# Kernel tuning notes

Hardware: AMD Instinct MI355X
Metric: run time of the kernel (lower is better)

The kernel has to match this reference:

```python
import jax, jax.numpy as jnp
import numpy as np

H = 16
D = 64
WIN = 512
THETA = 10000.0


def _rope(x):
    # x: [B, H, T, D]
    T = x.shape[2]
    inv = 1.0 / (THETA ** (jnp.arange(0, D, 2, dtype=jnp.float32) / D))  # [D/2]
    f = jnp.arange(T, dtype=jnp.float32)[:, None] * inv[None, :]          # [T, D/2]
    f = jnp.concatenate([f, f], axis=-1)                                  # [T, D]
    cos, sin = jnp.cos(f), jnp.sin(f)
    x1, x2 = jnp.split(x, 2, axis=-1)
    rot = jnp.concatenate([-x2, x1], axis=-1)
    return x * cos + rot * sin


def setup_inputs() -> dict:
    key = jax.random.key(0)
    ks = jax.random.split(key, 9)
    C = H * D
    s = 0.02
    return {
        "x":  jax.random.normal(ks[0], (2, 2048, C), dtype=jnp.float32),
        "Wq": jax.random.normal(ks[1], (C, C), dtype=jnp.float32) * s,
        "bq": jnp.zeros((C,), dtype=jnp.float32),
        "Wk": jax.random.normal(ks[2], (C, C), dtype=jnp.float32) * s,
        "bk": jnp.zeros((C,), dtype=jnp.float32),
        "Wv": jax.random.normal(ks[3], (C, C), dtype=jnp.float32) * s,
        "bv": jnp.zeros((C,), dtype=jnp.float32),
        "Wo": jax.random.normal(ks[4], (C, C), dtype=jnp.float32) * s,
        "bo": jnp.zeros((C,), dtype=jnp.float32),
    }


def reference(x, Wq, bq, Wk, bk, Wv, bv, Wo, bo):
    B, T, C = x.shape
    def split_heads(y):
        return y.reshape(B, T, H, D).transpose(0, 2, 1, 3)  # [B,H,T,D]
    q = split_heads(x @ Wq + bq)
    k = split_heads(x @ Wk + bk)
    v = split_heads(x @ Wv + bv)
    q = _rope(q)
    k = _rope(k)
    scores = jnp.einsum('bhqd,bhkd->bhqk', q, k) * (1.0 / np.sqrt(D))
    # the original module does NOT apply a causal mask, only the window).
    idx = jnp.arange(T)
    allowed = idx[None, :] >= idx[:, None] - (WIN - 1)      # [T, T] bool
    scores = jnp.where(allowed[None, None], scores, -jnp.inf)
    attn = jax.nn.softmax(scores, axis=-1)
    out = jnp.einsum('bhqk,bhkd->bhqd', attn, v)
    out = out.transpose(0, 2, 1, 3).reshape(B, T, C)
    return out @ Wo + bo
```

## Files before the change

kernel.cpp:

```cpp
#include <hip/hip_runtime.h>
#include <hip/hip_bf16.h>
#include <math.h>

#define Bsz 2
#define Tt  2048
#define Cc  1024
#define Hh  16
#define Dd  64

typedef __attribute__((ext_vector_type(8))) short short8v;
typedef __attribute__((ext_vector_type(4))) short short4v;
typedef __attribute__((ext_vector_type(8))) _Float16 half8v;
typedef __attribute__((ext_vector_type(4))) float f32x4;
typedef __attribute__((ext_vector_type(16))) float f32x16;
typedef __attribute__((ext_vector_type(4))) unsigned int uint4v;

static __device__ __forceinline__ short f2h(float f) {
  _Float16 h = (_Float16)f;
  return __builtin_bit_cast(short, h);
}
static __device__ __forceinline__ float h2f(short s) {
  _Float16 h = __builtin_bit_cast(_Float16, s);
  return (float)h;
}
static __device__ __forceinline__ void gll16(const void* g, void* l) {
  __builtin_amdgcn_global_load_lds((const __attribute__((address_space(1))) unsigned int*)g,
                                   (__attribute__((address_space(3))) unsigned int*)l, 16, 0, 0);
}

__global__ void cast_x(const float* __restrict__ x, short* __restrict__ xh) {
  int t = blockIdx.x * 256 + threadIdx.x;
  const float* s = x + (size_t)t * 8;
  float4 a = *(const float4*)s, b = *(const float4*)(s + 4);
  short8v h;
  h[0] = f2h(a.x); h[1] = f2h(a.y); h[2] = f2h(a.z); h[3] = f2h(a.w);
  h[4] = f2h(b.x); h[5] = f2h(b.y); h[6] = f2h(b.z); h[7] = f2h(b.w);
  *(short8v*)(xh + (size_t)t * 8) = h;
}

__global__ __launch_bounds__(256) void cast_wT(const float* __restrict__ Wq,
                                               const float* __restrict__ Wk,
                                               const float* __restrict__ Wv,
                                               const float* __restrict__ Wo,
                                               short* __restrict__ WTh) {
  __shared__ float T[64][68];
  const int z = blockIdx.z;
  const float* W = z == 0 ? Wq : z == 1 ? Wk : z == 2 ? Wv : Wo;
  short* oh = WTh + (size_t)z * 1048576;
  const int n0 = blockIdx.x * 64, k0 = blockIdx.y * 64;
  const int tid = threadIdx.x;
#pragma unroll
  for (int i = 0; i < 4; ++i) {
    int slot = tid + i * 256;
    int r = slot >> 4, c4 = (slot & 15) << 2;
    *(float4*)&T[r][c4] = *(const float4*)(W + (size_t)(k0 + r) * Cc + n0 + c4);
  }
  __syncthreads();
#pragma unroll
  for (int i = 0; i < 2; ++i) {
    int slot = tid + i * 256;
    int nl = slot >> 3, ks = (slot & 7) << 3;
    short8v h;
#pragma unroll
    for (int e = 0; e < 8; ++e) h[e] = f2h(T[ks + e][nl]);
    *(short8v*)(oh + (size_t)(n0 + nl) * Cc + k0 + ks) = h;
  }
}

__device__ __forceinline__ void core128h(const short* __restrict__ Ah,
                                         const short* __restrict__ Bh,
                                         short* AhL, short* BhL,
                                         int row0, int col0, int wv, int lane, f32x4 acc[4][4]) {
  const int l15 = lane & 15, g = lane >> 4;
  const int wr = wv >> 1, wc = wv & 1;

  const int srow0 = wv * 32 + (lane >> 2);
  const int srow1 = srow0 + 16;
  const int sch0 = ((lane & 3) ^ ((lane >> 2) & 3)) << 3;
  const size_t aoff0 = (size_t)(row0 + srow0) * Cc + sch0;
  const size_t aoff1 = (size_t)(row0 + srow1) * Cc + sch0;
  const size_t boff0 = (size_t)(col0 + srow0) * Cc + sch0;
  const size_t boff1 = (size_t)(col0 + srow1) * Cc + sch0;
  short* dA0 = AhL + wv * 1024;  short* dA1 = dA0 + 512;
  short* dB0 = BhL + wv * 1024;  short* dB1 = dB0 + 512;

  int aL[4], bL[4];
#pragma unroll
  for (int m = 0; m < 4; ++m) aL[m] = (wr * 64 + m * 16 + l15) * 32 + ((g ^ (l15 & 3)) << 3);
#pragma unroll
  for (int n = 0; n < 4; ++n) bL[n] = (wc * 64 + n * 16 + l15) * 32 + ((g ^ (l15 & 3)) << 3);

  for (int k0 = 0; k0 < Cc; k0 += 32) {
    __syncthreads();
    gll16(Ah + aoff0 + k0, dA0);
    gll16(Ah + aoff1 + k0, dA1);
    gll16(Bh + boff0 + k0, dB0);
    gll16(Bh + boff1 + k0, dB1);
    __syncthreads();
    half8v a[4], b[4];
#pragma unroll
    for (int m = 0; m < 4; ++m) a[m] = __builtin_bit_cast(half8v, *(short8v*)&AhL[aL[m]]);
#pragma unroll
    for (int n = 0; n < 4; ++n) b[n] = __builtin_bit_cast(half8v, *(short8v*)&BhL[bL[n]]);
#pragma unroll
    for (int m = 0; m < 4; ++m)
#pragma unroll
      for (int n = 0; n < 4; ++n)
        acc[m][n] = __builtin_amdgcn_mfma_f32_16x16x32_f16(a[m], b[n], acc[m][n], 0, 0, 0);
  }
}

__global__ __launch_bounds__(256, 3) void gemm_qkv(const short* __restrict__ xh,
                                                   const short* __restrict__ WTh,
                                                   const float* __restrict__ bq,
                                                   const float* __restrict__ bk,
                                                   const float* __restrict__ bv,
                                                   short* __restrict__ qb,
                                                   short* __restrict__ kb,
                                                   short* __restrict__ vb) {
  __shared__ short AhL[4096], BhL[4096];
  const int mode = blockIdx.y;
  const short* Bh = WTh + (size_t)mode * 1048576;
  const float* bias = mode == 0 ? bq : mode == 1 ? bk : bv;
  short* Y = mode == 0 ? qb : mode == 1 ? kb : vb;

  const int bid = blockIdx.x;
  const int nid = ((bid & 7) << 5) | (bid >> 3);
  const int row0 = (nid >> 3) * 128, col0 = (nid & 7) * 128;
  const int lane = threadIdx.x & 63, wv = threadIdx.x >> 6;
  const int l15 = lane & 15, g = lane >> 4;
  const int wr = wv >> 1, wc = wv & 1;

  f32x4 acc[4][4];
#pragma unroll
  for (int m = 0; m < 4; ++m)
#pragma unroll
    for (int n = 0; n < 4; ++n) acc[m][n] = (f32x4){0.f, 0.f, 0.f, 0.f};

  core128h(xh, Bh, AhL, BhL, row0, col0, wv, lane, acc);

  const int cbase = col0 + wc * 64;
  const int h = cbase >> 6;
  if (mode < 2) {
    const float scale = (mode == 0) ? 0.18033688f : 1.0f;
#pragma unroll
    for (int n = 0; n < 2; ++n) {
      const int d = n * 16 + l15;
      const float b0 = bias[cbase + d], b1 = bias[cbase + d + 32];
      const float inv = exp2f(-(float)d * (13.2877123795494f / 32.f));
#pragma unroll
      for (int m = 0; m < 4; ++m)
#pragma unroll
        for (int rr = 0; rr < 4; ++rr) {
          int R = row0 + wr * 64 + m * 16 + g * 4 + rr;
          int bI = R >> 11, t = R & (Tt - 1);
          float sn, cs;
          sincosf((float)t * inv, &sn, &cs);
          float v0 = acc[m][n][rr] + b0, v1 = acc[m][n + 2][rr] + b1;
          size_t base = (((size_t)(bI * Hh + h) * Tt + t) << 6) + d;
          Y[base]      = f2h((v0 * cs - v1 * sn) * scale);
          Y[base + 32] = f2h((v1 * cs + v0 * sn) * scale);
        }
    }
  } else {
#pragma unroll
    for (int n = 0; n < 2; ++n) {
      const int d = n * 16 + l15;
      const float b0 = bias[cbase + d], b1 = bias[cbase + d + 32];
#pragma unroll
      for (int m = 0; m < 4; ++m) {
        int R = row0 + wr * 64 + m * 16 + g * 4;
        int bI = R >> 11, t = R & (Tt - 1);
        short4v s0, s1;
#pragma unroll
        for (int rr = 0; rr < 4; ++rr) {
          s0[rr] = f2h(acc[m][n][rr] + b0);
          s1[rr] = f2h(acc[m][n + 2][rr] + b1);
        }
        size_t base = ((size_t)(bI * Hh + h) * Dd);
        *(short4v*)(Y + (base + d) * Tt + t)      = s0;
        *(short4v*)(Y + (base + d + 32) * Tt + t) = s1;
      }
    }
  }
}

__global__ __launch_bounds__(256, 3) void gemm_out(const short* __restrict__ ah,
                                                   const short* __restrict__ WTo,
                                                   const float* __restrict__ bias,
                                                   float* __restrict__ Y) {
  __shared__ short AhL[4096], BhL[4096];
  const int bid = blockIdx.x;
  const int nid = ((bid & 7) << 5) | (bid >> 3);
  const int row0 = (nid >> 3) * 128, col0 = (nid & 7) * 128;
  const int lane = threadIdx.x & 63, wv = threadIdx.x >> 6;
  const int l15 = lane & 15, g = lane >> 4;
  const int wr = wv >> 1, wc = wv & 1;

  f32x4 acc[4][4];
#pragma unroll
  for (int m = 0; m < 4; ++m)
#pragma unroll
    for (int n = 0; n < 4; ++n) acc[m][n] = (f32x4){0.f, 0.f, 0.f, 0.f};

  core128h(ah, WTo, AhL, BhL, row0, col0, wv, lane, acc);

  const int cbase = col0 + wc * 64;
#pragma unroll
  for (int n = 0; n < 2; ++n) {
    const int ccol = cbase + n * 16 + l15;
    const float b0 = bias[ccol], b1 = bias[ccol + 32];
#pragma unroll
    for (int m = 0; m < 4; ++m)
#pragma unroll
      for (int rr = 0; rr < 4; ++rr) {
        int R = row0 + wr * 64 + m * 16 + g * 4 + rr;
        Y[(size_t)R * Cc + ccol]      = acc[m][n][rr] + b0;
        Y[(size_t)R * Cc + ccol + 32] = acc[m][n + 2][rr] + b1;
      }
  }
}

static __device__ const int JQ[27] = {11, 0,0, 1,1, 2,2, 3,3, 4,4, 12, 5,5,
                                      6,6, 13, 7,7, 8,8, 14, 9,9, 15, 10,10};
static __device__ const int JK[27] = {0, 0,1, 0,1, 0,1, 0,1, 0,1, 0, 0,1,
                                      0,1, 0, 0,1, 0,1, 0, 0,1, 0, 0,1};

__global__ __launch_bounds__(256, 4) void attn_mfma(const short* __restrict__ q,
                                                    const short* __restrict__ k,
                                                    const short* __restrict__ vT,
                                                    short* __restrict__ ah,
                                                    float* __restrict__ yb,
                                                    float* __restrict__ side) {
  const int n = blockIdx.x;
  const int xcd = n & 7;
  const int t7 = n >> 3;
  const int bhj = t7 / 27;
  const int j = t7 - bhj * 27;
  const int bh = xcd * 4 + bhj;
  const int Q = JQ[j];
  const int kh = JK[j];
  const int split = (Q <= 10);
  const int q0 = Q * 128;

  const int tid = threadIdx.x;
  const int lane = tid & 63;
  const int wv = tid >> 6;
  const int l31 = lane & 31;
  const int hb = lane >> 5;
  const int qbase = q0 + wv * 32;
  const int tq = qbase + l31;

  const short* qgb = q + (size_t)bh * Tt * Dd;
  const short* kgb = k + (size_t)bh * Tt * Dd;
  const short* vgb = vT + (size_t)bh * Dd * Tt;

  const short* qp = qgb + (size_t)tq * Dd + 8 * hb;
  half8v qf[4];
#pragma unroll
  for (int i = 0; i < 4; ++i) qf[i] = __builtin_bit_cast(half8v, *(const short8v*)(qp + 16 * i));

  __shared__ short Klds[2][32 * 64];
  __shared__ short Vt[2][64 * 32];

  const int r8 = lane >> 3;
  const size_t ksrc_off = (size_t)(wv * 8 + r8) * Dd + (((lane & 7) ^ r8) << 3);

  const int vlog = ((lane & 3) - ((lane >> 3) & 3)) & 3;
  const size_t vsrc_off = (size_t)(wv * 16 + (lane >> 2)) * Tt + 8 * vlog;

  int koff[4];
#pragma unroll
  for (int i = 0; i < 4; ++i) koff[i] = l31 * 64 + (((2 * i + hb) ^ (l31 & 7)) << 3);
  const int rsw = (l31 >> 1) & 3;
  const int p0 = (hb + rsw) & 3;
  const int p1 = (2 + hb + rsw) & 3;
  const int voff00 = l31 * 32 + p0 * 8;
  const int voff01 = l31 * 32 + p1 * 8;
  const int voff10 = (32 + l31) * 32 + p0 * 8;
  const int voff11 = (32 + l31) * 32 + p1 * 8;

  f32x16 oacc[2];
#pragma unroll
  for (int t = 0; t < 2; ++t)
#pragma unroll
    for (int r = 0; r < 16; ++r) oacc[t][r] = 0.f;
  float lrun = 0.f;

  const int cs0 = (q0 >= 512) ? (q0 - 511) : 0;
  const int cstart = cs0 & ~31;
  const int nch_b = (Tt - cstart) >> 5;
  const int lower = (nch_b + 1) >> 1;
  const int mystart = cstart + ((split && kh) ? (lower << 5) : 0);
  const int myn = split ? (kh ? nch_b - lower : lower) : nch_b;

  gll16(kgb + (size_t)mystart * Dd + ksrc_off, &Klds[0][wv * 512]);
  gll16(vgb + vsrc_off + mystart, &Vt[0][wv * 512]);
  __syncthreads();

  for (int ci = 0; ci < myn; ++ci) {
    const int jt = mystart + (ci << 5);
    const int cur = ci & 1;

    if (ci + 1 < myn) {
      gll16(kgb + (size_t)(jt + 32) * Dd + ksrc_off, &Klds[cur ^ 1][wv * 512]);
      gll16(vgb + vsrc_off + (jt + 32), &Vt[cur ^ 1][wv * 512]);
    }

    const short* kbuf = &Klds[cur][0];
    f32x16 se;
#pragma unroll
    for (int r = 0; r < 16; ++r) se[r] = 0.f;
#pragma unroll
    for (int i = 0; i < 4; ++i) {
      half8v kf = __builtin_bit_cast(half8v, *(short8v*)&kbuf[koff[i]]);
      se = __builtin_amdgcn_mfma_f32_32x32x16_f16(kf, qf[i], se, 0, 0, 0);
    }

    if (jt < qbase - 480) {
      int th = tq - 511 - jt;
#pragma unroll
      for (int r = 0; r < 16; ++r) {
        int row = (r & 3) + 8 * (r >> 2) + 4 * hb;
        if (row < th) se[r] = -1e30f;
      }
    }

    float p[16], psum = 0.f;
#pragma unroll
    for (int r = 0; r < 16; ++r) { p[r] = exp2f(se[r]); psum += p[r]; }
    psum += __shfl_xor(psum, 32);
    lrun += psum;

    unsigned pk[8];
#pragma unroll
    for (int i = 0; i < 8; ++i)
      pk[i] = __builtin_bit_cast(unsigned, __builtin_amdgcn_cvt_pkrtz(p[2 * i], p[2 * i + 1]));
    asm volatile("v_permlane32_swap_b32 %0, %1" : "+v"(pk[0]), "+v"(pk[2]));
    asm volatile("v_permlane32_swap_b32 %0, %1" : "+v"(pk[1]), "+v"(pk[3]));
    asm volatile("v_permlane32_swap_b32 %0, %1" : "+v"(pk[4]), "+v"(pk[6]));
    asm volatile("v_permlane32_swap_b32 %0, %1" : "+v"(pk[5]), "+v"(pk[7]));
    uint4v f0, f1;
    f0[0] = pk[0]; f0[1] = pk[1]; f0[2] = pk[2]; f0[3] = pk[3];
    f1[0] = pk[4]; f1[1] = pk[5]; f1[2] = pk[6]; f1[3] = pk[7];
    half8v pf0 = __builtin_bit_cast(half8v, f0);
    half8v pf1 = __builtin_bit_cast(half8v, f1);

    half8v v00 = __builtin_bit_cast(half8v, *(short8v*)&Vt[cur][voff00]);
    half8v v01 = __builtin_bit_cast(half8v, *(short8v*)&Vt[cur][voff01]);
    half8v v10 = __builtin_bit_cast(half8v, *(short8v*)&Vt[cur][voff10]);
    half8v v11 = __builtin_bit_cast(half8v, *(short8v*)&Vt[cur][voff11]);
    oacc[0] = __builtin_amdgcn_mfma_f32_32x32x16_f16(v00, pf0, oacc[0], 0, 0, 0);
    oacc[0] = __builtin_amdgcn_mfma_f32_32x32x16_f16(v01, pf1, oacc[0], 0, 0, 0);
    oacc[1] = __builtin_amdgcn_mfma_f32_32x32x16_f16(v10, pf0, oacc[1], 0, 0, 0);
    oacc[1] = __builtin_amdgcn_mfma_f32_32x32x16_f16(v11, pf1, oacc[1], 0, 0, 0);

    __syncthreads();
  }

  const float invl = 1.f / lrun;
  const int row = bh * Tt + tq;
  if (split && hb == 0) side[kh * 65536 + row] = lrun;
  const int bI = bh >> 4, hd = bh & 15;
  if (!split || kh == 0) {
    short* op = ah + ((size_t)(bI * Tt + tq)) * Cc + hd * Dd;
#pragma unroll
    for (int t = 0; t < 2; ++t)
#pragma unroll
      for (int rq = 0; rq < 4; ++rq) {
        short4v hv;
#pragma unroll
        for (int rr = 0; rr < 4; ++rr) hv[rr] = f2h(oacc[t][4 * rq + rr] * invl);
        *(short4v*)(op + 32 * t + 8 * rq + 4 * hb) = hv;
      }
  } else {
    float* yp = yb + (size_t)row * 64;
#pragma unroll
    for (int t = 0; t < 2; ++t)
#pragma unroll
      for (int rq = 0; rq < 4; ++rq) {
        f32x4 o4;
#pragma unroll
        for (int rr = 0; rr < 4; ++rr) o4[rr] = oacc[t][4 * rq + rr] * invl;
        *(f32x4*)(yp + 32 * t + 8 * rq + 4 * hb) = o4;
      }
  }
}

__global__ __launch_bounds__(256) void attn_merge(short* __restrict__ ah,
                                                  const float* __restrict__ yb,
                                                  const float* __restrict__ side) {
  const int bh = blockIdx.y;
  const int idx = blockIdx.x * 256 + threadIdx.x;
  const int tq = idx >> 2;
  const int qd = (idx & 3) << 4;
  const int row = bh * Tt + tq;
  const float l0 = side[row], l1 = side[65536 + row];
  const float inv = 1.f / (l0 + l1);
  const float a0 = l0 * inv, a1 = l1 * inv;

  const int bI = bh >> 4, hd = bh & 15;
  short* op = ah + ((size_t)(bI * Tt + tq)) * Cc + hd * Dd + qd;
  const float* yp = yb + (size_t)row * 64 + qd;

  short8v h0 = *(short8v*)op, h1 = *(short8v*)(op + 8);
  short8v o0, o1;
#pragma unroll
  for (int e = 0; e < 8; ++e) o0[e] = f2h(a0 * h2f(h0[e]) + a1 * yp[e]);
#pragma unroll
  for (int e = 0; e < 8; ++e) o1[e] = f2h(a0 * h2f(h1[e]) + a1 * yp[8 + e]);
  *(short8v*)op = o0;
  *(short8v*)(op + 8) = o1;
}

extern "C" void kernel_launch(void* const* d_in, const int* in_sizes, int n_in,
                              void* d_out, int out_size, void* d_ws, size_t ws_size,
                              hipStream_t stream) {
  const float* x  = (const float*)d_in[0];
  const float* Wq = (const float*)d_in[1];
  const float* bq = (const float*)d_in[2];
  const float* Wk = (const float*)d_in[3];
  const float* bk = (const float*)d_in[4];
  const float* Wv = (const float*)d_in[5];
  const float* bv = (const float*)d_in[6];
  const float* Wo = (const float*)d_in[7];
  const float* bo = (const float*)d_in[8];

  short* ws16 = (short*)d_ws;
  short* xh  = ws16;
  short* WTh = ws16 + 4194304;
  short* qb  = ws16 + 8388608;
  short* kb  = ws16 + 12582912;
  short* vb  = ws16 + 16777216;
  short* ah  = ws16 + 20971520;
  float* yb   = (float*)(ws16 + 25165824);
  float* side = yb + 4194304;

  cast_x<<<2048, 256, 0, stream>>>(x, xh);
  cast_wT<<<dim3(16, 16, 4), 256, 0, stream>>>(Wq, Wk, Wv, Wo, WTh);

  gemm_qkv<<<dim3(256, 3), 256, 0, stream>>>(xh, WTh, bq, bk, bv, qb, kb, vb);

  attn_mfma<<<864, 256, 0, stream>>>(qb, kb, vb, ah, yb, side);
  attn_merge<<<dim3(22, 32), 256, 0, stream>>>(ah, yb, side);

  gemm_out<<<256, 256, 0, stream>>>(ah, WTh + 3 * 1048576, bo, (float*)d_out);
}
```

Baseline: 135.0 us.

## Triple-buffer K/V LDS tiles with two-ahead prefetch and explicit waitcnt

Expands the K and V shared-memory buffers from two to three stages and issues global-to-LDS loads two chunks ahead. The block-wide __syncthreads is replaced by explicit vmcnt waits plus s_barrier and sched_barrier, so loads can stay in flight longer. MFMA sections are also bracketed with s_setprio to raise wave priority during matrix work. This costs more LDS per block, which may lower occupancy, and relies on the hand-written vmcnt counts being correct.

```diff
diff --git a/kernel.cpp b/kernel.cpp
--- a/kernel.cpp
+++ b/kernel.cpp
@@ -260,8 +260,8 @@
 #pragma unroll
   for (int i = 0; i < 4; ++i) qf[i] = __builtin_bit_cast(half8v, *(const short8v*)(qp + 16 * i));
 
-  __shared__ short Klds[2][32 * 64];
-  __shared__ short Vt[2][64 * 32];
+  __shared__ short Klds[3][2048];
+  __shared__ short Vt[3][2048];
 
   const int r8 = lane >> 3;
   const size_t ksrc_off = (size_t)(wv * 8 + r8) * Dd + (((lane & 7) ^ r8) << 3);
@@ -296,26 +296,38 @@
 
   gll16(kgb + (size_t)mystart * Dd + ksrc_off, &Klds[0][wv * 512]);
   gll16(vgb + vsrc_off + mystart, &Vt[0][wv * 512]);
-  __syncthreads();
-
+  if (myn > 1) {
+    gll16(kgb + (size_t)(mystart + 32) * Dd + ksrc_off, &Klds[1][wv * 512]);
+    gll16(vgb + vsrc_off + mystart + 32, &Vt[1][wv * 512]);
+    asm volatile("s_waitcnt vmcnt(2)" ::: "memory");
+  } else {
+    asm volatile("s_waitcnt vmcnt(0)" ::: "memory");
+  }
+  __builtin_amdgcn_s_barrier();
+  __builtin_amdgcn_sched_barrier(0);
+
+  int s0 = 0, s1 = 1, s2 = 2;
   for (int ci = 0; ci < myn; ++ci) {
     const int jt = mystart + (ci << 5);
-    const int cur = ci & 1;
-
-    if (ci + 1 < myn) {
-      gll16(kgb + (size_t)(jt + 32) * Dd + ksrc_off, &Klds[cur ^ 1][wv * 512]);
-      gll16(vgb + vsrc_off + (jt + 32), &Vt[cur ^ 1][wv * 512]);
-    }
-
-    const short* kbuf = &Klds[cur][0];
+    const bool more = (ci + 2 < myn);
+
+    if (more) {
+      gll16(kgb + (size_t)(jt + 64) * Dd + ksrc_off, &Klds[s2][wv * 512]);
+      gll16(vgb + vsrc_off + (jt + 64), &Vt[s2][wv * 512]);
+    }
+    __builtin_amdgcn_sched_barrier(0);
+
+    const short* kbuf = &Klds[s0][0];
     f32x16 se;
 #pragma unroll
     for (int r = 0; r < 16; ++r) se[r] = 0.f;
+    __builtin_amdgcn_s_setprio(1);
 #pragma unroll
     for (int i = 0; i < 4; ++i) {
       half8v kf = __builtin_bit_cast(half8v, *(short8v*)&kbuf[koff[i]]);
       se = __builtin_amdgcn_mfma_f32_32x32x16_f16(kf, qf[i], se, 0, 0, 0);
     }
+    __builtin_amdgcn_s_setprio(0);
 
     if (jt < qbase - 480) {
       int th = tq - 511 - jt;
@@ -346,16 +358,24 @@
     half8v pf0 = __builtin_bit_cast(half8v, f0);
     half8v pf1 = __builtin_bit_cast(half8v, f1);
 
-    half8v v00 = __builtin_bit_cast(half8v, *(short8v*)&Vt[cur][voff00]);
-    half8v v01 = __builtin_bit_cast(half8v, *(short8v*)&Vt[cur][voff01]);
-    half8v v10 = __builtin_bit_cast(half8v, *(short8v*)&Vt[cur][voff10]);
-    half8v v11 = __builtin_bit_cast(half8v, *(short8v*)&Vt[cur][voff11]);
+    half8v v00 = __builtin_bit_cast(half8v, *(short8v*)&Vt[s0][voff00]);
+    half8v v01 = __builtin_bit_cast(half8v, *(short8v*)&Vt[s0][voff01]);
+    half8v v10 = __builtin_bit_cast(half8v, *(short8v*)&Vt[s0][voff10]);
+    half8v v11 = __builtin_bit_cast(half8v, *(short8v*)&Vt[s0][voff11]);
+    __builtin_amdgcn_s_setprio(1);
     oacc[0] = __builtin_amdgcn_mfma_f32_32x32x16_f16(v00, pf0, oacc[0], 0, 0, 0);
     oacc[0] = __builtin_amdgcn_mfma_f32_32x32x16_f16(v01, pf1, oacc[0], 0, 0, 0);
     oacc[1] = __builtin_amdgcn_mfma_f32_32x32x16_f16(v10, pf0, oacc[1], 0, 0, 0);
     oacc[1] = __builtin_amdgcn_mfma_f32_32x32x16_f16(v11, pf1, oacc[1], 0, 0, 0);
-
-    __syncthreads();
+    __builtin_amdgcn_s_setprio(0);
+
+    if (ci + 1 < myn) {
+      if (more) asm volatile("s_waitcnt vmcnt(2)" ::: "memory");
+      else      asm volatile("s_waitcnt vmcnt(0)" ::: "memory");
+      __builtin_amdgcn_s_barrier();
+      __builtin_amdgcn_sched_barrier(0);
+    }
+    int tmp = s0; s0 = s1; s1 = s2; s2 = tmp;
   }
 
   const float invl = 1.f / lrun;
```

Measured after the change: 136.1 us. No clear change (+0.8%).

## Split attention into single-wave blocks with per-wave K/V pipelines

Applied to the files above, without the earlier changes.

The attention kernel now launches one 64-thread wave per block (four times as many blocks) instead of four waves sharing a K/V tile. Each wave loads the whole 32-key K and V chunk into its own LDS double buffer. The block-wide __syncthreads is replaced by explicit vmcnt waits, and the MFMA sections are wrapped in s_setprio. This removes barrier stalls between waves and lets waves progress independently. In exchange each wave issues four times the global-to-LDS traffic, and more LDS per wave may limit occupancy.

```diff
diff --git a/kernel.cpp b/kernel.cpp
--- a/kernel.cpp
+++ b/kernel.cpp
@@ -226,29 +226,29 @@
 static __device__ const int JK[27] = {0, 0,1, 0,1, 0,1, 0,1, 0,1, 0, 0,1,
                                       0,1, 0, 0,1, 0,1, 0, 0,1, 0, 0,1};
 
-__global__ __launch_bounds__(256, 4) void attn_mfma(const short* __restrict__ q,
-                                                    const short* __restrict__ k,
-                                                    const short* __restrict__ vT,
-                                                    short* __restrict__ ah,
-                                                    float* __restrict__ yb,
-                                                    float* __restrict__ side) {
+__global__ __launch_bounds__(64, 4) void attn_mfma(const short* __restrict__ q,
+                                                   const short* __restrict__ k,
+                                                   const short* __restrict__ vT,
+                                                   short* __restrict__ ah,
+                                                   float* __restrict__ yb,
+                                                   float* __restrict__ side) {
   const int n = blockIdx.x;
   const int xcd = n & 7;
   const int t7 = n >> 3;
-  const int bhj = t7 / 27;
-  const int j = t7 - bhj * 27;
+  const int bhj = t7 / 108;
+  const int rem = t7 - bhj * 108;
+  const int j = rem >> 2;
+  const int qs = rem & 3;
   const int bh = xcd * 4 + bhj;
   const int Q = JQ[j];
   const int kh = JK[j];
   const int split = (Q <= 10);
   const int q0 = Q * 128;
 
-  const int tid = threadIdx.x;
-  const int lane = tid & 63;
-  const int wv = tid >> 6;
+  const int lane = threadIdx.x;
   const int l31 = lane & 31;
   const int hb = lane >> 5;
-  const int qbase = q0 + wv * 32;
+  const int qbase = q0 + qs * 32;
   const int tq = qbase + l31;
 
   const short* qgb = q + (size_t)bh * Tt * Dd;
@@ -260,14 +260,12 @@
 #pragma unroll
   for (int i = 0; i < 4; ++i) qf[i] = __builtin_bit_cast(half8v, *(const short8v*)(qp + 16 * i));
 
-  __shared__ short Klds[2][32 * 64];
-  __shared__ short Vt[2][64 * 32];
-
-  const int r8 = lane >> 3;
-  const size_t ksrc_off = (size_t)(wv * 8 + r8) * Dd + (((lane & 7) ^ r8) << 3);
-
+  __shared__ short Klds[2][2048];
+  __shared__ short Vt[2][2048];
+
+  const int ksrc = (lane >> 3) * Dd + (((lane & 7) ^ (lane >> 3)) << 3);
   const int vlog = ((lane & 3) - ((lane >> 3) & 3)) & 3;
-  const size_t vsrc_off = (size_t)(wv * 16 + (lane >> 2)) * Tt + 8 * vlog;
+  const int vsrc = (lane >> 2) * Tt + 8 * vlog;
 
   int koff[4];
 #pragma unroll
@@ -294,28 +292,39 @@
   const int mystart = cstart + ((split && kh) ? (lower << 5) : 0);
   const int myn = split ? (kh ? nch_b - lower : lower) : nch_b;
 
-  gll16(kgb + (size_t)mystart * Dd + ksrc_off, &Klds[0][wv * 512]);
-  gll16(vgb + vsrc_off + mystart, &Vt[0][wv * 512]);
-  __syncthreads();
-
+#pragma unroll
+  for (int g = 0; g < 4; ++g) {
+    gll16(kgb + (size_t)mystart * Dd + g * 8 * Dd + ksrc, &Klds[0][g * 512]);
+    gll16(vgb + (size_t)g * 16 * Tt + vsrc + mystart, &Vt[0][g * 512]);
+  }
+
+  int cur = 0;
   for (int ci = 0; ci < myn; ++ci) {
     const int jt = mystart + (ci << 5);
-    const int cur = ci & 1;
 
     if (ci + 1 < myn) {
-      gll16(kgb + (size_t)(jt + 32) * Dd + ksrc_off, &Klds[cur ^ 1][wv * 512]);
-      gll16(vgb + vsrc_off + (jt + 32), &Vt[cur ^ 1][wv * 512]);
+#pragma unroll
+      for (int g = 0; g < 4; ++g) {
+        gll16(kgb + (size_t)(jt + 32) * Dd + g * 8 * Dd + ksrc, &Klds[cur ^ 1][g * 512]);
+        gll16(vgb + (size_t)g * 16 * Tt + vsrc + (jt + 32), &Vt[cur ^ 1][g * 512]);
+      }
+      asm volatile("s_waitcnt vmcnt(8)" ::: "memory");
+    } else {
+      asm volatile("s_waitcnt vmcnt(0)" ::: "memory");
     }
+    __builtin_amdgcn_sched_barrier(0);
 
     const short* kbuf = &Klds[cur][0];
     f32x16 se;
 #pragma unroll
     for (int r = 0; r < 16; ++r) se[r] = 0.f;
+    __builtin_amdgcn_s_setprio(1);
 #pragma unroll
     for (int i = 0; i < 4; ++i) {
       half8v kf = __builtin_bit_cast(half8v, *(short8v*)&kbuf[koff[i]]);
       se = __builtin_amdgcn_mfma_f32_32x32x16_f16(kf, qf[i], se, 0, 0, 0);
     }
+    __builtin_amdgcn_s_setprio(0);
 
     if (jt < qbase - 480) {
       int th = tq - 511 - jt;
@@ -350,12 +359,14 @@
     half8v v01 = __builtin_bit_cast(half8v, *(short8v*)&Vt[cur][voff01]);
     half8v v10 = __builtin_bit_cast(half8v, *(short8v*)&Vt[cur][voff10]);
     half8v v11 = __builtin_bit_cast(half8v, *(short8v*)&Vt[cur][voff11]);
+    __builtin_amdgcn_s_setprio(1);
     oacc[0] = __builtin_amdgcn_mfma_f32_32x32x16_f16(v00, pf0, oacc[0], 0, 0, 0);
     oacc[0] = __builtin_amdgcn_mfma_f32_32x32x16_f16(v01, pf1, oacc[0], 0, 0, 0);
     oacc[1] = __builtin_amdgcn_mfma_f32_32x32x16_f16(v10, pf0, oacc[1], 0, 0, 0);
     oacc[1] = __builtin_amdgcn_mfma_f32_32x32x16_f16(v11, pf1, oacc[1], 0, 0, 0);
-
-    __syncthreads();
+    __builtin_amdgcn_s_setprio(0);
+
+    cur ^= 1;
   }
 
   const float invl = 1.f / lrun;
@@ -441,7 +452,7 @@
 
   gemm_qkv<<<dim3(256, 3), 256, 0, stream>>>(xh, WTh, bq, bk, bv, qb, kb, vb);
 
-  attn_mfma<<<864, 256, 0, stream>>>(qb, kb, vb, ah, yb, side);
+  attn_mfma<<<3456, 64, 0, stream>>>(qb, kb, vb, ah, yb, side);
   attn_merge<<<dim3(22, 32), 256, 0, stream>>>(ah, yb, side);
 
   gemm_out<<<256, 256, 0, stream>>>(ah, WTh + 3 * 1048576, bo, (float*)d_out);
```

Result: slower. 153.8 us (+14.0%).
